# Optimization experiments

Hardware: AMD Instinct MI355X
Metric: run time of the kernel (lower is better)

Reference implementation:

```python
import jax, jax.numpy as jnp
import numpy as np
from jax import lax


def setup_inputs() -> dict:
    key = jax.random.key(0)
    k1, k2, k3 = jax.random.split(key, 3)
    B, K, H, W = 16, 11, 128, 128
    pred = jax.random.normal(k1, (B, K * 7, H, W), dtype=jnp.float32)
    gt = jax.random.normal(k2, (B, K, 7), dtype=jnp.float32)
    heatmap = jax.random.normal(k3, (B, K, H, W), dtype=jnp.float32)
    return {"pred": pred, "gt": gt, "heatmap": heatmap}


def reference(pred, gt, heatmap):
    B, K, H, W = heatmap.shape
    # AvgPool2d(kernel=3, stride=1, pad=1), count_include_pad=True (torch default) -> divide by 9 everywhere
    pooled = lax.reduce_window(
        heatmap, 0.0, lax.add,
        window_dimensions=(1, 1, 3, 3),
        window_strides=(1, 1, 1, 1),
        padding=((0, 0), (0, 0), (1, 1), (1, 1)),
    ) / 9.0
    # per (batch, gt-box) argmax over flattened HxW map
    index = jnp.argmax(pooled.reshape(B, K, H * W), axis=-1)  # [B, K]
    m = H  # faithful to original: x = index // m, y = index % m with m = size[2]
    x = index // m
    y = index % m
    # gather pred[b, k*7:(k+1)*7, x, y]
    predk = pred.reshape(B, K, 7, H, W)
    b_idx = jnp.arange(B)[:, None, None]          # [B,1,1]
    k_idx = jnp.arange(K)[None, :, None]          # [1,K,1]
    c_idx = jnp.arange(7)[None, None, :]          # [1,1,7]
    vals = predk[b_idx, k_idx, c_idx, x[..., None], y[..., None]]  # [B,K,7]
    diff = vals - gt[:, :, :7]
    class_loss = jnp.sum(diff * diff, axis=-1)    # MSE(reduction='sum') per (b,k)
    return class_loss.mean(axis=1)                # [B]
```

## Files before the change

### kernel.cpp

```cpp
#include <hip/hip_runtime.h>

#define HW    128
#define NPIX  16384
#define KBOX  11
#define NCH   7
#define NBLK  256

__global__ __launch_bounds__(NBLK) void label_loss_kernel(
    const float* __restrict__ pred,
    const float* __restrict__ gt,
    const float* __restrict__ heatmap,
    float* __restrict__ out)
{
    __shared__ float sm[NPIX];
    __shared__ float wv[4];
    __shared__ int   wi[4];

    const int bk  = blockIdx.x;
    const int b   = bk / KBOX;
    const int k   = bk % KBOX;
    const int tid = threadIdx.x;

    const float4* src = (const float4*)(heatmap + (size_t)bk * NPIX);
    float4* dst = (float4*)sm;
    #pragma unroll
    for (int i = tid; i < NPIX / 4; i += NBLK) dst[i] = src[i];
    __syncthreads();

    float best = -INFINITY;
    int bestIdx = 0;
    for (int p = tid; p < NPIX; p += NBLK) {
        const int r = p >> 7;
        const int c = p & 127;
        float s = 0.f;
        #pragma unroll
        for (int dr = -1; dr <= 1; ++dr) {
            const int rr = r + dr;
            if ((unsigned)rr < (unsigned)HW) {
                const float* row = sm + (rr << 7);
                s += row[c];
                if (c > 0)      s += row[c - 1];
                if (c < HW - 1) s += row[c + 1];
            }
        }
        s *= (1.f / 9.f);
        if (s > best) { best = s; bestIdx = p; }
    }

    #pragma unroll
    for (int off = 32; off > 0; off >>= 1) {
        const float ov = __shfl_down(best, off, 64);
        const int   oi = __shfl_down(bestIdx, off, 64);
        if (ov > best || (ov == best && oi < bestIdx)) { best = ov; bestIdx = oi; }
    }
    const int wave = tid >> 6;
    if ((tid & 63) == 0) { wv[wave] = best; wi[wave] = bestIdx; }
    __syncthreads();

    if (tid == 0) {
        best = wv[0]; bestIdx = wi[0];
        #pragma unroll
        for (int w = 1; w < NBLK / 64; ++w) {
            if (wv[w] > best || (wv[w] == best && wi[w] < bestIdx)) {
                best = wv[w]; bestIdx = wi[w];
            }
        }
        const float* pbase = pred + ((size_t)(b * (KBOX * NCH) + k * NCH)) * NPIX + bestIdx;
        const float* gbase = gt + (size_t)(b * KBOX + k) * NCH;
        float loss = 0.f;
        #pragma unroll
        for (int c = 0; c < NCH; ++c) {
            const float d = pbase[(size_t)c * NPIX] - gbase[c];
            loss += d * d;
        }
        atomicAdd(out + b, loss * (1.0f / KBOX));
    }
}

extern "C" void kernel_launch(void* const* d_in, const int* in_sizes, int n_in,
                              void* d_out, int out_size, void* d_ws, size_t ws_size,
                              hipStream_t stream) {
    const float* pred    = (const float*)d_in[0];
    const float* gt      = (const float*)d_in[1];
    const float* heatmap = (const float*)d_in[2];
    float* out = (float*)d_out;

    hipMemsetAsync(out, 0, (size_t)out_size * sizeof(float), stream);

    label_loss_kernel<<<dim3(16 * KBOX), dim3(NBLK), 0, stream>>>(pred, gt, heatmap, out);
}
```

Measured before the change: 139.2 us.

## Split pooling argmax into row tiles and add a separate gather-loss kernel

Each heatmap is now split into 4 row tiles of 32 rows plus halo, one block per tile, which raises the grid from 176 to 704 blocks and cuts shared memory per block from 64KB to about 17KB. Per-tile argmax candidates go to workspace, and a second single-block kernel merges them, gathers the 7 pred values and sums the per-batch losses. This drops the memset and the atomics. In exchange it adds a second kernel launch and re-reads 2 halo rows per tile.

```diff
diff --git a/kernel.cpp b/kernel.cpp
--- a/kernel.cpp
+++ b/kernel.cpp
@@ -4,47 +4,56 @@
 #define NPIX  16384
 #define KBOX  11
 #define NCH   7
+#define NMAP  176
+#define TILES 4
+#define TROWS 32
 #define NBLK  256
 
-__global__ __launch_bounds__(NBLK) void label_loss_kernel(
-    const float* __restrict__ pred,
-    const float* __restrict__ gt,
+__global__ __launch_bounds__(NBLK) void pool_argmax_kernel(
     const float* __restrict__ heatmap,
-    float* __restrict__ out)
+    float* __restrict__ wsv, int* __restrict__ wsi)
 {
-    __shared__ float sm[NPIX];
-    __shared__ float wv[4];
-    __shared__ int   wi[4];
+    __shared__ float sm[(TROWS + 2) * HW];
+    __shared__ float wv[NBLK / 64];
+    __shared__ int   wi[NBLK / 64];
 
-    const int bk  = blockIdx.x;
-    const int b   = bk / KBOX;
-    const int k   = bk % KBOX;
-    const int tid = threadIdx.x;
+    const int bk   = blockIdx.x;
+    const int tile = blockIdx.y;
+    const int tid  = threadIdx.x;
+    const int r0   = tile * TROWS;
 
-    const float4* src = (const float4*)(heatmap + (size_t)bk * NPIX);
-    float4* dst = (float4*)sm;
-    #pragma unroll
-    for (int i = tid; i < NPIX / 4; i += NBLK) dst[i] = src[i];
+    const float* base = heatmap + (size_t)bk * NPIX;
+
+    for (int i = tid; i < ((TROWS + 2) * HW) / 4; i += NBLK) {
+        const int l  = i * 4;
+        const int lr = l >> 7;
+        const int gr = r0 - 1 + lr;
+        float4 v;
+        if ((unsigned)gr < (unsigned)HW)
+            v = *(const float4*)(base + ((size_t)gr << 7) + (l & 127));
+        else
+            v = make_float4(0.f, 0.f, 0.f, 0.f);
+        *(float4*)(sm + l) = v;
+    }
     __syncthreads();
 
     float best = -INFINITY;
     int bestIdx = 0;
-    for (int p = tid; p < NPIX; p += NBLK) {
-        const int r = p >> 7;
-        const int c = p & 127;
+    #pragma unroll
+    for (int i = 0; i < (TROWS * HW) / NBLK; ++i) {
+        const int p  = tid + i * NBLK;
+        const int lr = p >> 7;
+        const int c  = p & 127;
         float s = 0.f;
         #pragma unroll
-        for (int dr = -1; dr <= 1; ++dr) {
-            const int rr = r + dr;
-            if ((unsigned)rr < (unsigned)HW) {
-                const float* row = sm + (rr << 7);
-                s += row[c];
-                if (c > 0)      s += row[c - 1];
-                if (c < HW - 1) s += row[c + 1];
-            }
+        for (int dr = 0; dr < 3; ++dr) {
+            const float* row = sm + ((lr + dr) << 7);
+            s += row[c];
+            if (c > 0)      s += row[c - 1];
+            if (c < HW - 1) s += row[c + 1];
         }
         s *= (1.f / 9.f);
-        if (s > best) { best = s; bestIdx = p; }
+        if (s > best) { best = s; bestIdx = (r0 + lr) * HW + c; }
     }
 
     #pragma unroll
@@ -65,15 +74,47 @@
                 best = wv[w]; bestIdx = wi[w];
             }
         }
-        const float* pbase = pred + ((size_t)(b * (KBOX * NCH) + k * NCH)) * NPIX + bestIdx;
-        const float* gbase = gt + (size_t)(b * KBOX + k) * NCH;
+        wsv[bk * TILES + tile] = best;
+        wsi[bk * TILES + tile] = bestIdx;
+    }
+}
+
+__global__ __launch_bounds__(NBLK) void gather_loss_kernel(
+    const float* __restrict__ pred, const float* __restrict__ gt,
+    const float* __restrict__ wsv, const int* __restrict__ wsi,
+    float* __restrict__ out)
+{
+    __shared__ float losses[NMAP];
+    const int t = threadIdx.x;
+
+    if (t < NMAP) {
+        float best = wsv[t * TILES];
+        int   bi   = wsi[t * TILES];
+        #pragma unroll
+        for (int s = 1; s < TILES; ++s) {
+            const float v = wsv[t * TILES + s];
+            const int   j = wsi[t * TILES + s];
+            if (v > best || (v == best && j < bi)) { best = v; bi = j; }
+        }
+        const int b = t / KBOX;
+        const int k = t % KBOX;
+        const float* pb = pred + (size_t)(b * (KBOX * NCH) + k * NCH) * NPIX + bi;
+        const float* gb = gt + (size_t)t * NCH;
         float loss = 0.f;
         #pragma unroll
         for (int c = 0; c < NCH; ++c) {
-            const float d = pbase[(size_t)c * NPIX] - gbase[c];
+            const float d = pb[(size_t)c * NPIX] - gb[c];
             loss += d * d;
         }
-        atomicAdd(out + b, loss * (1.0f / KBOX));
+        losses[t] = loss;
+    }
+    __syncthreads();
+
+    if (t < NMAP / KBOX) {
+        float s = 0.f;
+        #pragma unroll
+        for (int k = 0; k < KBOX; ++k) s += losses[t * KBOX + k];
+        out[t] = s * (1.0f / KBOX);
     }
 }
 
@@ -85,7 +126,9 @@
     const float* heatmap = (const float*)d_in[2];
     float* out = (float*)d_out;
 
-    hipMemsetAsync(out, 0, (size_t)out_size * sizeof(float), stream);
+    float* wsv = (float*)d_ws;
+    int*   wsi = (int*)((float*)d_ws + NMAP * TILES);
 
-    label_loss_kernel<<<dim3(16 * KBOX), dim3(NBLK), 0, stream>>>(pred, gt, heatmap, out);
+    pool_argmax_kernel<<<dim3(NMAP, TILES), dim3(NBLK), 0, stream>>>(heatmap, wsv, wsi);
+    gather_loss_kernel<<<dim3(1), dim3(NBLK), 0, stream>>>(pred, gt, wsv, wsi, out);
 }
```

Result: faster. 121.1 us (-13.0%).
